# Performance work log

Hardware: AMD Instinct MI355X
Metric: run time of the kernel (lower is better)

Reference implementation:

```python
import jax, jax.numpy as jnp
import numpy as np

B, F, NQ, DT, TS, K = 16384, 256, 2048, 256, 16, 8
GH, SH, CALH = 128, 128, 16
SPD = DT + TS
SPH = max(int(SPD * 0.25), 16)
CD = DT + 3 + TS + 3  # h_base + y_base + 3 gate stats + z_top + |d_safe| + |d_spec| = 278
CH = max(int(CD * 0.25), 16)
RES_SCALE = 0.1


def _ln(x, g, b):
    m = x.mean(-1, keepdims=True)
    v = ((x - m) ** 2).mean(-1, keepdims=True)
    return (x - m) * jax.lax.rsqrt(v + 1e-5) * g + b


def _resmlp(x, lg, lb, w1, b1, w2, b2):
    h = jnp.maximum(_ln(x, lg, lb) @ w1 + b1, 0.0)
    return h @ w2 + b2


def setup_inputs() -> dict:
    key = jax.random.key(0)
    ks = iter(jax.random.split(key, 48))
    def nrm(shape, s=0.05):
        return jax.random.normal(next(ks), shape, jnp.float32) * s
    d = {}
    d["x_num"] = jax.random.normal(next(ks), (B, F), jnp.float32)
    d["robust_center"] = nrm((1, F), 0.1)
    d["robust_scale"] = jax.random.uniform(next(ks), (1, F), jnp.float32, 0.5, 1.5)
    d["quantile_sorted"] = jnp.sort(jax.random.normal(next(ks), (NQ, F), jnp.float32), axis=0)
    d["stem_w1"] = nrm((3, CALH)); d["stem_b1"] = jnp.zeros((CALH,))
    d["stem_w2"] = nrm((CALH, CALH)); d["stem_b2"] = jnp.zeros((CALH,))
    d["stem_w3"] = nrm((CALH, 1)); d["stem_b3"] = jnp.zeros((1,))
    d["gate_w1"] = nrm((F, GH)); d["gate_b1"] = jnp.zeros((GH,))
    d["gate_w2"] = nrm((GH, F)); d["gate_b2"] = jnp.zeros((F,))
    d["bb_w"] = nrm((F, DT)); d["bb_b"] = jnp.zeros((DT,))
    d["base_w"] = nrm((DT, 1)); d["base_b"] = jnp.zeros((1,))
    d["safe_lg"] = jnp.ones((DT,)); d["safe_lb"] = jnp.zeros((DT,))
    d["safe_w1"] = nrm((DT, SH)); d["safe_b1"] = jnp.zeros((SH,))
    d["safe_w2"] = nrm((SH, 1)); d["safe_b2"] = jnp.zeros((1,))
    d["top_w1"] = nrm((1, TS)); d["top_b1"] = jnp.zeros((TS,))
    d["top_w2"] = nrm((TS, TS)); d["top_b2"] = jnp.zeros((TS,))
    d["spec_lg"] = jnp.ones((SPD,)); d["spec_lb"] = jnp.zeros((SPD,))
    d["spec_w1"] = nrm((SPD, SPH)); d["spec_b1"] = jnp.zeros((SPH,))
    d["spec_w2"] = nrm((SPH, 1)); d["spec_b2"] = jnp.zeros((1,))
    d["conf_lg"] = jnp.ones((CD,)); d["conf_lb"] = jnp.zeros((CD,))
    d["conf_w1"] = nrm((CD, CH)); d["conf_b1"] = jnp.zeros((CH,))
    d["conf_w2"] = nrm((CH, 1)); d["conf_b2"] = jnp.full((1,), -2.0)  # gamma_init_bias
    return d


def _forward(x_num, robust_center, robust_scale, quantile_sorted,
             stem_w1, stem_b1, stem_w2, stem_b2, stem_w3, stem_b3,
             gate_w1, gate_b1, gate_w2, gate_b2,
             bb_w, bb_b, base_w, base_b,
             safe_lg, safe_lb, safe_w1, safe_b1, safe_w2, safe_b2,
             top_w1, top_b1, top_w2, top_b2,
             spec_lg, spec_lb, spec_w1, spec_b1, spec_w2, spec_b2,
             conf_lg, conf_lb, conf_w1, conf_b1, conf_w2, conf_b2):
    # --- calibration views ---
    x_robust = (x_num - robust_center) / robust_scale
    ranks = jax.vmap(jnp.searchsorted, in_axes=(1, 1), out_axes=1)(
        jax.lax.stop_gradient(quantile_sorted), jax.lax.stop_gradient(x_num))  # [B,F] int
    x_quant = jnp.clip(ranks.astype(jnp.float32) / (NQ - 1.0), 0.0, 1.0)
    x_views = jnp.stack([x_num, x_robust, x_quant], axis=-1)  # [B,F,3]
    h = jnp.maximum(x_views @ stem_w1 + stem_b1, 0.0)
    h = jnp.maximum(h @ stem_w2 + stem_b2, 0.0)
    resid = jnp.tanh((h @ stem_w3 + stem_b3)[..., 0])
    x_cal = x_num + RES_SCALE * resid
    # --- input gate ---
    g = jax.nn.sigmoid(jnp.maximum(x_cal @ gate_w1 + gate_b1, 0.0) @ gate_w2 + gate_b2)
    x_gated = x_cal * g
    # --- backbone (stand-in for TMLPBackbone.encode_hidden) ---
    h_base = jnp.maximum(x_gated @ bb_w + bb_b, 0.0)  # [B,DT]
    y_base = h_base @ base_w + base_b  # [B,1]
    gate_mean = g.mean(axis=1, keepdims=True)
    gate_max = g.max(axis=1, keepdims=True)
    gate_std = g.std(axis=1, keepdims=True)  # ddof=0, matches unbiased=False
    delta_safe = _resmlp(h_base, safe_lg, safe_lb, safe_w1, safe_b1, safe_w2, safe_b2)
    # --- top-k feature gather ---
    topk_g, topk_idx = jax.lax.top_k(g, K)
    topk_x = jnp.take_along_axis(x_cal, topk_idx, axis=1)
    topk_w = topk_g / (topk_g.sum(axis=1, keepdims=True) + 1e-6)
    xw = (topk_x * topk_w)[..., None]  # [B,K,1]
    tok = jnp.maximum(xw @ top_w1 + top_b1, 0.0) @ top_w2 + top_b2  # [B,K,TS]
    z_top = tok.mean(axis=1)  # [B,TS]
    delta_spec = _resmlp(jnp.concatenate([h_base, z_top], axis=1),
                         spec_lg, spec_lb, spec_w1, spec_b1, spec_w2, spec_b2)
    conf_in = jnp.concatenate([h_base, y_base, gate_mean, gate_max, gate_std,
                               z_top, jnp.abs(delta_safe), jnp.abs(delta_spec)], axis=1)
    gamma = jax.nn.sigmoid(_resmlp(conf_in, conf_lg, conf_lb, conf_w1, conf_b1, conf_w2, conf_b2))
    return (y_base + delta_safe + gamma * delta_spec)[:, 0]


def reference(x_num, robust_center, robust_scale, quantile_sorted,
              stem_w1, stem_b1, stem_w2, stem_b2, stem_w3, stem_b3,
              gate_w1, gate_b1, gate_w2, gate_b2,
              bb_w, bb_b, base_w, base_b,
              safe_lg, safe_lb, safe_w1, safe_b1, safe_w2, safe_b2,
              top_w1, top_b1, top_w2, top_b2,
              spec_lg, spec_lb, spec_w1, spec_b1, spec_w2, spec_b2,
              conf_lg, conf_lb, conf_w1, conf_b1, conf_w2, conf_b2):
    return _forward(x_num, robust_center, robust_scale, quantile_sorted,
                    stem_w1, stem_b1, stem_w2, stem_b2, stem_w3, stem_b3,
                    gate_w1, gate_b1, gate_w2, gate_b2,
                    bb_w, bb_b, base_w, base_b,
                    safe_lg, safe_lb, safe_w1, safe_b1, safe_w2, safe_b2,
                    top_w1, top_b1, top_w2, top_b2,
                    spec_lg, spec_lb, spec_w1, spec_b1, spec_w2, spec_b2,
                    conf_lg, conf_lb, conf_w1, conf_b1, conf_w2, conf_b2)
```

## Files before the change

kernel.cpp:

```cpp
#include <hip/hip_runtime.h>
#include <hip/hip_bf16.h>
#include <math.h>

static constexpr int B  = 16384;
static constexpr int F  = 256;
static constexpr int NQ = 2048;
static constexpr int TS = 16;
static constexpr int KTOP = 8;
static constexpr int SPD = 272;
static constexpr int SPH = 68;
static constexpr int CD  = 278;
static constexpr int CH  = 69;

typedef __attribute__((ext_vector_type(8))) short bf16x8;
typedef __attribute__((ext_vector_type(4))) float f32x4;
typedef _Float16 f16x2 __attribute__((ext_vector_type(2)));
typedef unsigned u32x4 __attribute__((ext_vector_type(4)));

__device__ inline short f2bf(float f) {
    unsigned u = __builtin_bit_cast(unsigned, f);
    unsigned r = (u + 0x7FFF + ((u >> 16) & 1)) >> 16;
    return (short)r;
}

__device__ inline unsigned pkbf(float a, float b) {
    __hip_bfloat162 h = __float22bfloat162_rn(make_float2(a, b));
    unsigned u;
    __builtin_memcpy(&u, &h, 4);
    return u;
}

__device__ inline float fast_tanh(float o) {
    o = fminf(fmaxf(o, -15.0f), 15.0f);
    float e = __expf(2.0f * o);
    return (e - 1.0f) / (e + 1.0f);
}

__device__ inline f16x2 cvt2h(float a, float b) {
    return __builtin_bit_cast(f16x2, __builtin_amdgcn_cvt_pkrtz(a, b));
}

__device__ inline unsigned pack2h(float a, float b) {
    return __builtin_bit_cast(unsigned, __builtin_amdgcn_cvt_pkrtz(a, b));
}

__device__ inline void prep_one(const float* W, short* T, int local,
                                int K, int N, int KP) {
    const int n = local / KP, k = local - n * KP;
    T[local] = (k < K && n < N) ? f2bf(W[k * N + n]) : (short)0;
}

__global__ __launch_bounds__(256) void k_prepall(
    const float* __restrict__ gate_w1, const float* __restrict__ gate_w2,
    const float* __restrict__ bb_w,    const float* __restrict__ safe_w1,
    const float* __restrict__ spec_w1, const float* __restrict__ conf_w1,
    const float* __restrict__ qs,
    const float* __restrict__ stem_w2, const float* __restrict__ stem_w3,
    short* __restrict__ w1t, short* __restrict__ w2t, short* __restrict__ bbt,
    short* __restrict__ sw1t, short* __restrict__ spw1t, short* __restrict__ cfw1t,
    float* __restrict__ qs_t,
    unsigned* __restrict__ w2ph, unsigned* __restrict__ w3ph)
{
    __shared__ float tile[64][65];
    if (blockIdx.x < 929) {
        const int idx = blockIdx.x * 256 + threadIdx.x;
        if (idx < 32768)       prep_one(gate_w1, w1t,  idx,           256, 128, 256);
        else if (idx < 65536)  prep_one(gate_w2, w2t,  idx - 32768,   128, 256, 128);
        else if (idx < 131072) prep_one(bb_w,    bbt,  idx - 65536,   256, 256, 256);
        else if (idx < 163840) prep_one(safe_w1, sw1t, idx - 131072,  256, 128, 256);
        else if (idx < 200704) prep_one(spec_w1, spw1t, idx - 163840, 272, 68, 288);
        else if (idx < 237568) prep_one(conf_w1, cfw1t, idx - 200704, 278, 69, 288);
        else if (idx < 237696) {
            const int l = idx - 237568;
            const int t = l >> 4, j = l & 15;
            w2ph[l] = pack2h(stem_w2[(2 * t) * 16 + j], stem_w2[(2 * t + 1) * 16 + j]);
        }
        else if (idx < 237704) {
            const int u = idx - 237696;
            w3ph[u] = pack2h(stem_w3[2 * u], stem_w3[2 * u + 1]);
        }
    } else {
        const int t = blockIdx.x - 929;
        const int tq = t & 31, tf = t >> 5;
        const int q0 = tq * 64, f0 = tf * 64;
        const int c = threadIdx.x & 63, r4 = threadIdx.x >> 6;
#pragma unroll
        for (int rr = 0; rr < 16; ++rr) {
            const int row = rr * 4 + r4;
            tile[row][c] = qs[(q0 + row) * 256 + f0 + c];
        }
        __syncthreads();
#pragma unroll
        for (int rr = 0; rr < 16; ++rr) {
            const int fr = rr * 4 + r4;
            qs_t[(long)(f0 + fr) * 2048 + q0 + c] = tile[c][fr];
        }
    }
}

__global__ __launch_bounds__(256) void k_calib7(
    const float* __restrict__ x_num, const float* __restrict__ center,
    const float* __restrict__ scale, const float* __restrict__ qs,
    const float* __restrict__ qs_t,
    const float* __restrict__ sw1, const float* __restrict__ sb1,
    const unsigned* __restrict__ w2ph, const float* __restrict__ sb2,
    const unsigned* __restrict__ w3ph, const float* __restrict__ sb3,
    float* __restrict__ x_cal)
{
    __shared__ float cq[63 * 256];
    const int tid = threadIdx.x;
    const int f = tid;
#pragma unroll 1
    for (int j0 = 0; j0 < 63; j0 += 9) {
        float t[9];
#pragma unroll
        for (int u = 0; u < 9; ++u) t[u] = qs[(32 * (j0 + u + 1)) * 256 + tid];
#pragma unroll
        for (int u = 0; u < 9; ++u) cq[(j0 + u) * 256 + tid] = t[u];
    }
    __syncthreads();

    const float c = center[f];
    const float inv_sc = 1.0f / scale[f];
    const float* colp = qs_t + (long)f * NQ;
    const long row_base = (long)blockIdx.x * 32;

    float xb[8];
#pragma unroll
    for (int i = 0; i < 8; ++i) xb[i] = x_num[(row_base + i) * F + f];

#pragma unroll
    for (int grp = 0; grp < 4; ++grp) {
        const long r0 = row_base + grp * 8;
        float x[8], xr[8];
#pragma unroll
        for (int i = 0; i < 8; ++i) x[i] = xb[i];
        if (grp < 3) {
#pragma unroll
            for (int i = 0; i < 8; ++i) xb[i] = x_num[(r0 + 8 + i) * F + f];
        }
#pragma unroll
        for (int i = 0; i < 8; ++i) xr[i] = (x[i] - c) * inv_sc;

        int lo[8], hi[8];
#pragma unroll
        for (int i = 0; i < 8; ++i) { lo[i] = 0; hi[i] = 63; }
#pragma unroll
        for (int it = 0; it < 6; ++it) {
            float qv[8]; int mid[8];
#pragma unroll
            for (int i = 0; i < 8; ++i) {
                mid[i] = (lo[i] + hi[i]) >> 1;
                qv[i] = cq[mid[i] * 256 + f];
            }
#pragma unroll
            for (int i = 0; i < 8; ++i) {
                if (qv[i] < x[i]) lo[i] = mid[i] + 1; else hi[i] = mid[i];
            }
        }
        int base[8];
        {
            float pm[8];
#pragma unroll
            for (int i = 0; i < 8; ++i) pm[i] = colp[lo[i] * 32 + 16];
#pragma unroll
            for (int i = 0; i < 8; ++i)
                base[i] = lo[i] * 32 + ((pm[i] < x[i]) ? 16 : 0);
        }
        float xq[8];
#pragma unroll
        for (int i = 0; i < 8; ++i) {
            const float4* wp = reinterpret_cast<const float4*>(&colp[base[i]]);
            const float4 a = wp[0], b = wp[1], d = wp[2], e = wp[3];
            int cN = 0;
            cN += (a.x < x[i]); cN += (a.y < x[i]); cN += (a.z < x[i]); cN += (a.w < x[i]);
            cN += (b.x < x[i]); cN += (b.y < x[i]); cN += (b.z < x[i]); cN += (b.w < x[i]);
            cN += (d.x < x[i]); cN += (d.y < x[i]); cN += (d.z < x[i]); cN += (d.w < x[i]);
            cN += (e.x < x[i]); cN += (e.y < x[i]); cN += (e.z < x[i]); cN += (e.w < x[i]);
            const int rank = base[i] + cN;
            xq[i] = fminf((float)rank * (1.0f / (float)(NQ - 1)), 1.0f);
        }

#pragma unroll
        for (int hgrp = 0; hgrp < 2; ++hgrp) {
            const int o4 = hgrp * 4;
            float h2[4][16];
#pragma unroll
            for (int j = 0; j < 16; ++j) {
                const float bb = sb2[j];
#pragma unroll
                for (int i = 0; i < 4; ++i) h2[i][j] = bb;
            }
#pragma unroll 4
            for (int t = 0; t < 8; ++t) {
                const float w0a = sw1[2 * t],     w1a = sw1[16 + 2 * t],     w2a = sw1[32 + 2 * t];
                const float w0b = sw1[2 * t + 1], w1b = sw1[16 + 2 * t + 1], w2b = sw1[32 + 2 * t + 1];
                const float ba = sb1[2 * t], bbv = sb1[2 * t + 1];
                f16x2 hp[4];
#pragma unroll
                for (int i = 0; i < 4; ++i) {
                    const float ha = fmaxf(ba  + x[o4 + i] * w0a + xr[o4 + i] * w1a + xq[o4 + i] * w2a, 0.0f);
                    const float hb = fmaxf(bbv + x[o4 + i] * w0b + xr[o4 + i] * w1b + xq[o4 + i] * w2b, 0.0f);
                    hp[i] = cvt2h(ha, hb);
                }
                unsigned ww[16];
                const uint4* wr = reinterpret_cast<const uint4*>(&w2ph[t * 16]);
                *reinterpret_cast<uint4*>(&ww[0])  = wr[0];
                *reinterpret_cast<uint4*>(&ww[4])  = wr[1];
                *reinterpret_cast<uint4*>(&ww[8])  = wr[2];
                *reinterpret_cast<uint4*>(&ww[12]) = wr[3];
#pragma unroll
                for (int j = 0; j < 16; ++j) {
                    const f16x2 wj = __builtin_bit_cast(f16x2, ww[j]);
#pragma unroll
                    for (int i = 0; i < 4; ++i)
                        h2[i][j] = __builtin_amdgcn_fdot2(hp[i], wj, h2[i][j], false);
                }
            }
            const float b3 = sb3[0];
            float o[4] = {b3, b3, b3, b3};
#pragma unroll
            for (int u = 0; u < 8; ++u) {
                const f16x2 wu = __builtin_bit_cast(f16x2, w3ph[u]);
#pragma unroll
                for (int i = 0; i < 4; ++i) {
                    const f16x2 hh = cvt2h(
                        fmaxf(h2[i][2 * u], 0.0f), fmaxf(h2[i][2 * u + 1], 0.0f));
                    o[i] = __builtin_amdgcn_fdot2(hh, wu, o[i], false);
                }
            }
#pragma unroll
            for (int i = 0; i < 4; ++i)
                x_cal[(r0 + o4 + i) * F + f] = x[o4 + i] + 0.1f * fast_tanh(o[i]);
        }
    }
}

static constexpr int ST1 = 136;
static constexpr int ST2 = 264;

__global__ __launch_bounds__(256) void k_fused(
    const float* __restrict__ x_cal,
    const short* __restrict__ w1t, const float* __restrict__ gate_b1,
    const short* __restrict__ w2t, const float* __restrict__ gate_b2,
    const short* __restrict__ bbt, const float* __restrict__ bb_b,
    float* __restrict__ g, float* __restrict__ h_b)
{
    __shared__ short s_c1[32 * ST1];
    __shared__ short s_xg[32 * ST2];

    const int tid = threadIdx.x;
    const int wave = tid >> 6, lane = tid & 63;
    const int sub = lane & 15, quad = lane >> 4;
    const int wm = wave & 1, wn = wave >> 1;
    const long row0 = (long)blockIdx.x * 32;
    const long mrow = row0 + wm * 16 + sub;

    {
        f32x4 acc[4];
#pragma unroll
        for (int t = 0; t < 4; ++t) acc[t] = (f32x4){0, 0, 0, 0};
#pragma unroll
        for (int k0 = 0; k0 < 256; k0 += 32) {
            const float* ap = x_cal + mrow * 256 + k0 + quad * 8;
            float av[8];
            *reinterpret_cast<float4*>(&av[0]) = *reinterpret_cast<const float4*>(ap);
            *reinterpret_cast<float4*>(&av[4]) = *reinterpret_cast<const float4*>(ap + 4);
            u32x4 afu;
            afu[0] = pkbf(av[0], av[1]);
            afu[1] = pkbf(av[2], av[3]);
            afu[2] = pkbf(av[4], av[5]);
            afu[3] = pkbf(av[6], av[7]);
            const bf16x8 af = __builtin_bit_cast(bf16x8, afu);
#pragma unroll
            for (int t = 0; t < 4; ++t) {
                const int col = wn * 64 + t * 16 + sub;
                const bf16x8 bf = *reinterpret_cast<const bf16x8*>(
                    &w1t[(long)col * 256 + k0 + quad * 8]);
                acc[t] = __builtin_amdgcn_mfma_f32_16x16x32_bf16(af, bf, acc[t], 0, 0, 0);
            }
        }
#pragma unroll
        for (int t = 0; t < 4; ++t) {
            const int col = wn * 64 + t * 16 + sub;
            const float bb = gate_b1[col];
#pragma unroll
            for (int r = 0; r < 4; ++r) {
                const int rowl = wm * 16 + quad * 4 + r;
                s_c1[rowl * ST1 + col] = f2bf(fmaxf(acc[t][r] + bb, 0.0f));
            }
        }
    }
    __syncthreads();

    {
        f32x4 acc[8];
#pragma unroll
        for (int t = 0; t < 8; ++t) acc[t] = (f32x4){0, 0, 0, 0};
#pragma unroll
        for (int k0 = 0; k0 < 128; k0 += 32) {
            const bf16x8 af = *reinterpret_cast<const bf16x8*>(
                &s_c1[(wm * 16 + sub) * ST1 + k0 + quad * 8]);
#pragma unroll
            for (int t = 0; t < 8; ++t) {
                const int col = wn * 128 + t * 16 + sub;
                const bf16x8 bf = *reinterpret_cast<const bf16x8*>(
                    &w2t[(long)col * 128 + k0 + quad * 8]);
                acc[t] = __builtin_amdgcn_mfma_f32_16x16x32_bf16(af, bf, acc[t], 0, 0, 0);
            }
        }
#pragma unroll
        for (int t = 0; t < 8; ++t) {
            const int col = wn * 128 + t * 16 + sub;
            const float bb = gate_b2[col];
#pragma unroll
            for (int r = 0; r < 4; ++r) {
                const int rowl = wm * 16 + quad * 4 + r;
                const float gv = 1.0f / (1.0f + __expf(-(acc[t][r] + bb)));
                g[(row0 + rowl) * 256 + col] = gv;
                const float xg = x_cal[(row0 + rowl) * 256 + col] * gv;
                s_xg[rowl * ST2 + col] = f2bf(xg);
            }
        }
    }
    __syncthreads();

    {
        f32x4 acc[8];
#pragma unroll
        for (int t = 0; t < 8; ++t) acc[t] = (f32x4){0, 0, 0, 0};
#pragma unroll
        for (int k0 = 0; k0 < 256; k0 += 32) {
            const bf16x8 af = *reinterpret_cast<const bf16x8*>(
                &s_xg[(wm * 16 + sub) * ST2 + k0 + quad * 8]);
#pragma unroll
            for (int t = 0; t < 8; ++t) {
                const int col = wn * 128 + t * 16 + sub;
                const bf16x8 bf = *reinterpret_cast<const bf16x8*>(
                    &bbt[(long)col * 256 + k0 + quad * 8]);
                acc[t] = __builtin_amdgcn_mfma_f32_16x16x32_bf16(af, bf, acc[t], 0, 0, 0);
            }
        }
#pragma unroll
        for (int t = 0; t < 8; ++t) {
            const int col = wn * 128 + t * 16 + sub;
            const float bb = bb_b[col];
#pragma unroll
            for (int r = 0; r < 4; ++r) {
                const int rowl = wm * 16 + quad * 4 + r;
                h_b[(row0 + rowl) * 256 + col] = fmaxf(acc[t][r] + bb, 0.0f);
            }
        }
    }
}

__global__ __launch_bounds__(256) void k_topk(
    const float* __restrict__ g, const float* __restrict__ x_cal,
    const float* __restrict__ tw1, const float* __restrict__ tb1,
    const float* __restrict__ tw2, const float* __restrict__ tb2,
    float* __restrict__ z_top, float* __restrict__ stats)
{
    __shared__ float s_hm[4][16];
    const int wave = threadIdx.x >> 6;
    const int lane = threadIdx.x & 63;
    const int b = blockIdx.x * 4 + wave;
    const long base = (long)b * F;

    float gv[4];
#pragma unroll
    for (int i = 0; i < 4; ++i) gv[i] = g[base + lane + 64 * i];

    float s = gv[0] + gv[1] + gv[2] + gv[3];
    float mx = fmaxf(fmaxf(gv[0], gv[1]), fmaxf(gv[2], gv[3]));
    for (int m = 32; m; m >>= 1) {
        s  += __shfl_xor(s, m);
        mx  = fmaxf(mx, __shfl_xor(mx, m));
    }
    const float mean = s * (1.0f / 256.0f);
    float vs = 0.0f;
#pragma unroll
    for (int i = 0; i < 4; ++i) { float d = gv[i] - mean; vs += d * d; }
    for (int m = 32; m; m >>= 1) vs += __shfl_xor(vs, m);
    const float stdv = sqrtf(vs * (1.0f / 256.0f));

    float cur[4]; int curi[4];
#pragma unroll
    for (int i = 0; i < 4; ++i) { cur[i] = gv[i]; curi[i] = lane + 64 * i; }
    float tv[KTOP]; int ti[KTOP]; float vsum = 0.0f;
    for (int r = 0; r < KTOP; ++r) {
        float bv = cur[0]; int bi = curi[0];
#pragma unroll
        for (int i = 1; i < 4; ++i)
            if (cur[i] > bv || (cur[i] == bv && curi[i] < bi)) { bv = cur[i]; bi = curi[i]; }
        for (int m = 32; m; m >>= 1) {
            float ov = __shfl_xor(bv, m);
            int   oi = __shfl_xor(bi, m);
            if (ov > bv || (ov == bv && oi < bi)) { bv = ov; bi = oi; }
        }
        tv[r] = bv; ti[r] = bi; vsum += bv;
#pragma unroll
        for (int i = 0; i < 4; ++i) if (curi[i] == bi) cur[i] = -INFINITY;
    }
    const float denom = 1.0f / (vsum + 1e-6f);

    if (lane < 16) {
        float hm = 0.0f;
        for (int k = 0; k < KTOP; ++k) {
            const float xk = x_cal[base + ti[k]];
            const float xw = xk * (tv[k] * denom);
            hm += fmaxf(xw * tw1[lane] + tb1[lane], 0.0f);
        }
        s_hm[wave][lane] = hm * (1.0f / (float)KTOP);
    }
    __syncthreads();
    if (lane < 16) {
        float z = tb2[lane];
#pragma unroll
        for (int j = 0; j < 16; ++j) z += s_hm[wave][j] * tw2[j * 16 + lane];
        z_top[(long)b * TS + lane] = z;
    }
    if (lane == 0) {
        stats[(long)b * 4 + 0] = mean;
        stats[(long)b * 4 + 1] = mx;
        stats[(long)b * 4 + 2] = stdv;
    }
}

static constexpr int HST = 260;
static constexpr int AST = 312;

template<int KP>
__device__ __forceinline__ void head_mfma16(
    const short* sa, const short* __restrict__ Wt,
    const float* __restrict__ b1v, const float* __restrict__ w2v, int Nreal,
    float (*s_red)[16], int wave, int sub, int quad)
{
    f32x4 acc[2];
#pragma unroll
    for (int t = 0; t < 2; ++t) acc[t] = (f32x4){0, 0, 0, 0};
#pragma unroll
    for (int k0 = 0; k0 < KP; k0 += 32) {
        const bf16x8 af = *reinterpret_cast<const bf16x8*>(
            &sa[sub * AST + k0 + quad * 8]);
#pragma unroll
        for (int t = 0; t < 2; ++t) {
            const int col = wave * 32 + t * 16 + sub;
            const bf16x8 bf = *reinterpret_cast<const bf16x8*>(
                &Wt[(long)col * KP + k0 + quad * 8]);
            acc[t] = __builtin_amdgcn_mfma_f32_16x16x32_bf16(af, bf, acc[t], 0, 0, 0);
        }
    }
    float rsum[4] = {0, 0, 0, 0};
#pragma unroll
    for (int t = 0; t < 2; ++t) {
        const int col = wave * 32 + t * 16 + sub;
        const float bb = (col < Nreal) ? b1v[col] : 0.0f;
        const float ww = (col < Nreal) ? w2v[col] : 0.0f;
#pragma unroll
        for (int rr = 0; rr < 4; ++rr)
            rsum[rr] += fmaxf(acc[t][rr] + bb, 0.0f) * ww;
    }
#pragma unroll
    for (int rr = 0; rr < 4; ++rr)
        for (int m = 1; m < 16; m <<= 1) rsum[rr] += __shfl_xor(rsum[rr], m);
    if (sub == 0) {
#pragma unroll
        for (int rr = 0; rr < 4; ++rr)
            s_red[wave][quad * 4 + rr] = rsum[rr];
    }
}

__global__ __launch_bounds__(256) void k_tail3(
    const float* __restrict__ h_base, const float* __restrict__ z_top,
    const float* __restrict__ gstats,
    const float* __restrict__ base_w, const float* __restrict__ base_b,
    const float* __restrict__ safe_lg, const float* __restrict__ safe_lb,
    const short* __restrict__ sw1t, const float* __restrict__ safe_b1,
    const float* __restrict__ safe_w2, const float* __restrict__ safe_b2,
    const float* __restrict__ spec_lg, const float* __restrict__ spec_lb,
    const short* __restrict__ spw1t, const float* __restrict__ spec_b1,
    const float* __restrict__ spec_w2, const float* __restrict__ spec_b2,
    const float* __restrict__ conf_lg, const float* __restrict__ conf_lb,
    const short* __restrict__ cfw1t, const float* __restrict__ conf_b1,
    const float* __restrict__ conf_w2, const float* __restrict__ conf_b2,
    float* __restrict__ out)
{
    __shared__ float s_h[16 * HST];
    __shared__ short s_a[16 * AST];
    __shared__ float s_z[16 * 16];
    __shared__ float s_g[16 * 4];
    __shared__ float s_sc[16 * 14];
    __shared__ float s_red[4][16];

    const int tid = threadIdx.x;
    const int wave = tid >> 6, lane = tid & 63;
    const int sub = lane & 15, quad = lane >> 4;
    const long row0 = (long)blockIdx.x * 16;

    for (int idx = tid; idx < 16 * 64; idx += 256) {
        const int r = idx >> 6, q = idx & 63;
        *reinterpret_cast<float4*>(&s_h[r * HST + q * 4]) =
            *reinterpret_cast<const float4*>(&h_base[(row0 + r) * 256 + q * 4]);
    }
    if (tid < 256) s_z[tid] = z_top[row0 * 16 + tid];
    if (tid < 64) s_g[tid] = gstats[row0 * 4 + tid];
    __syncthreads();

    {
        const int r = tid >> 4, l16 = tid & 15;
        float S = 0.0f, SS = 0.0f, Y = 0.0f;
#pragma unroll
        for (int i = 0; i < 16; ++i) {
            const int k = l16 + 16 * i;
            const float v = s_h[r * HST + k];
            S += v; SS += v * v; Y += v * base_w[k];
        }
        const float z0 = s_z[r * 16 + l16];
        float Sz = z0, SSz = z0 * z0;
#pragma unroll
        for (int m = 1; m < 16; m <<= 1) {
            S += __shfl_xor(S, m); SS += __shfl_xor(SS, m); Y += __shfl_xor(Y, m);
            Sz += __shfl_xor(Sz, m); SSz += __shfl_xor(SSz, m);
        }
        if (l16 == 0) {
            float* sc = &s_sc[r * 14];
            sc[0] = S; sc[1] = SS; sc[2] = Sz; sc[3] = SSz;
            sc[4] = Y + base_b[0];
            const float mu = S * (1.0f / 256.0f);
            sc[5] = mu;
            sc[6] = rsqrtf(SS * (1.0f / 256.0f) - mu * mu + 1e-5f);
            const float musp = (S + Sz) * (1.0f / (float)SPD);
            sc[7] = musp;
            sc[8] = rsqrtf((SS + SSz) * (1.0f / (float)SPD) - musp * musp + 1e-5f);
        }
    }
    __syncthreads();

    for (int idx = tid; idx < 16 * 128; idx += 256) {
        const int r = idx >> 7, k = (idx & 127) * 2;
        const float mu = s_sc[r * 14 + 5], rs = s_sc[r * 14 + 6];
        const float v0 = (s_h[r * HST + k] - mu) * rs * safe_lg[k] + safe_lb[k];
        const float v1 = (s_h[r * HST + k + 1] - mu) * rs * safe_lg[k + 1] + safe_lb[k + 1];
        *reinterpret_cast<unsigned*>(&s_a[r * AST + k]) = pkbf(v0, v1);
    }
    __syncthreads();

    head_mfma16<256>(s_a, sw1t, safe_b1, safe_w2, 128, s_red, wave, sub, quad);
    __syncthreads();

    if (tid < 16)
        s_sc[tid * 14 + 9] = s_red[0][tid] + s_red[1][tid] + s_red[2][tid] + s_red[3][tid] + safe_b2[0];
    for (int idx = tid; idx < 16 * 144; idx += 256) {
        const int r = idx / 144, k = (idx - r * 144) * 2;
        const float mu = s_sc[r * 14 + 7], rs = s_sc[r * 14 + 8];
        float vv[2];
#pragma unroll
        for (int h = 0; h < 2; ++h) {
            const int kk = k + h;
            float raw = (kk < 256) ? s_h[r * HST + kk]
                       : (kk < SPD) ? s_z[r * 16 + kk - 256] : 0.0f;
            vv[h] = (kk < SPD) ? (raw - mu) * rs * spec_lg[kk] + spec_lb[kk] : 0.0f;
        }
        *reinterpret_cast<unsigned*>(&s_a[r * AST + k]) = pkbf(vv[0], vv[1]);
    }
    __syncthreads();

    head_mfma16<288>(s_a, spw1t, spec_b1, spec_w2, SPH, s_red, wave, sub, quad);
    __syncthreads();

    if (tid < 16) {
        float* sc = &s_sc[tid * 14];
        const float dsp = s_red[0][tid] + s_red[1][tid] + s_red[2][tid] + s_red[3][tid] + spec_b2[0];
        sc[10] = dsp;
        const float yb = sc[4];
        const float gm = s_g[tid * 4 + 0], gx = s_g[tid * 4 + 1], gs = s_g[tid * 4 + 2];
        const float ads = fabsf(sc[9]), adp = fabsf(dsp);
        const float es = yb + gm + gx + gs + ads + adp;
        const float eq = yb * yb + gm * gm + gx * gx + gs * gs + ads * ads + adp * adp;
        const float muc = (sc[0] + sc[2] + es) * (1.0f / (float)CD);
        sc[11] = muc;
        sc[12] = rsqrtf((sc[1] + sc[3] + eq) * (1.0f / (float)CD) - muc * muc + 1e-5f);
    }
    __syncthreads();

    for (int idx = tid; idx < 16 * 144; idx += 256) {
        const int r = idx / 144, k = (idx - r * 144) * 2;
        const float mu = s_sc[r * 14 + 11], rs = s_sc[r * 14 + 12];
        float vv[2];
#pragma unroll
        for (int h = 0; h < 2; ++h) {
            const int kk = k + h;
            float raw;
            if (kk < 256)       raw = s_h[r * HST + kk];
            else if (kk == 256) raw = s_sc[r * 14 + 4];
            else if (kk == 257) raw = s_g[r * 4 + 0];
            else if (kk == 258) raw = s_g[r * 4 + 1];
            else if (kk == 259) raw = s_g[r * 4 + 2];
            else if (kk < 276)  raw = s_z[r * 16 + kk - 260];
            else if (kk == 276) raw = fabsf(s_sc[r * 14 + 9]);
            else if (kk == 277) raw = fabsf(s_sc[r * 14 + 10]);
            else                raw = 0.0f;
            vv[h] = (kk < CD) ? (raw - mu) * rs * conf_lg[kk] + conf_lb[kk] : 0.0f;
        }
        *reinterpret_cast<unsigned*>(&s_a[r * AST + k]) = pkbf(vv[0], vv[1]);
    }
    __syncthreads();

    head_mfma16<288>(s_a, cfw1t, conf_b1, conf_w2, CH, s_red, wave, sub, quad);
    __syncthreads();

    if (tid < 16) {
        const float* sc = &s_sc[tid * 14];
        const float gamma = 1.0f / (1.0f + __expf(
            -(s_red[0][tid] + s_red[1][tid] + s_red[2][tid] + s_red[3][tid] + conf_b2[0])));
        out[row0 + tid] = sc[4] + sc[9] + gamma * sc[10];
    }
}

extern "C" void kernel_launch(void* const* d_in, const int* in_sizes, int n_in,
                              void* d_out, int out_size, void* d_ws, size_t ws_size,
                              hipStream_t stream)
{
    const float* x_num   = (const float*)d_in[0];
    const float* center  = (const float*)d_in[1];
    const float* scale   = (const float*)d_in[2];
    const float* qs      = (const float*)d_in[3];
    const float* stem_w1 = (const float*)d_in[4];
    const float* stem_b1 = (const float*)d_in[5];
    const float* stem_w2 = (const float*)d_in[6];
    const float* stem_b2 = (const float*)d_in[7];
    const float* stem_w3 = (const float*)d_in[8];
    const float* stem_b3 = (const float*)d_in[9];
    const float* gate_w1 = (const float*)d_in[10];
    const float* gate_b1 = (const float*)d_in[11];
    const float* gate_w2 = (const float*)d_in[12];
    const float* gate_b2 = (const float*)d_in[13];
    const float* bb_w    = (const float*)d_in[14];
    const float* bb_b    = (const float*)d_in[15];
    const float* base_w  = (const float*)d_in[16];
    const float* base_b  = (const float*)d_in[17];
    const float* safe_lg = (const float*)d_in[18];
    const float* safe_lb = (const float*)d_in[19];
    const float* safe_w1 = (const float*)d_in[20];
    const float* safe_b1 = (const float*)d_in[21];
    const float* safe_w2 = (const float*)d_in[22];
    const float* safe_b2 = (const float*)d_in[23];
    const float* top_w1  = (const float*)d_in[24];
    const float* top_b1  = (const float*)d_in[25];
    const float* top_w2  = (const float*)d_in[26];
    const float* top_b2  = (const float*)d_in[27];
    const float* spec_lg = (const float*)d_in[28];
    const float* spec_lb = (const float*)d_in[29];
    const float* spec_w1 = (const float*)d_in[30];
    const float* spec_b1 = (const float*)d_in[31];
    const float* spec_w2 = (const float*)d_in[32];
    const float* spec_b2 = (const float*)d_in[33];
    const float* conf_lg = (const float*)d_in[34];
    const float* conf_lb = (const float*)d_in[35];
    const float* conf_w1 = (const float*)d_in[36];
    const float* conf_b1 = (const float*)d_in[37];
    const float* conf_w2 = (const float*)d_in[38];
    const float* conf_b2 = (const float*)d_in[39];

    float* ws    = (float*)d_ws;
    float* x_cal = ws;
    float* g_h   = x_cal + (long)B * 256;
    float* g     = g_h   + (long)B * 128;
    float* h_b   = g     + (long)B * 256;
    float* z_top = h_b   + (long)B * 256;
    float* gstat = z_top + (long)B * 16;
    short* w1t   = (short*)(gstat + (long)B * 4);
    short* w2t   = w1t   + 128 * 256;
    short* bbt   = w2t   + 256 * 128;
    short* sw1t  = bbt   + 256 * 256;
    short* spw1t = sw1t  + 128 * 256;
    short* cfw1t = spw1t + 128 * 288;
    unsigned* w2ph = (unsigned*)(cfw1t + 128 * 288);
    unsigned* w3ph = w2ph + 128;
    float* qs_t  = (float*)(w3ph + 8);
    float* out   = (float*)d_out;

    k_prepall<<<1057, 256, 0, stream>>>(gate_w1, gate_w2, bb_w, safe_w1, spec_w1,
                                        conf_w1, qs, stem_w2, stem_w3,
                                        w1t, w2t, bbt, sw1t, spw1t, cfw1t, qs_t,
                                        w2ph, w3ph);
    k_calib7<<<512, 256, 0, stream>>>(x_num, center, scale, qs, qs_t,
                                      stem_w1, stem_b1, w2ph, stem_b2, w3ph, stem_b3,
                                      x_cal);
    k_fused<<<512, 256, 0, stream>>>(x_cal, w1t, gate_b1, w2t, gate_b2, bbt, bb_b,
                                     g, h_b);
    k_topk<<<B / 4, 256, 0, stream>>>(g, x_cal, top_w1, top_b1, top_w2, top_b2, z_top, gstat);
    k_tail3<<<B / 16, 256, 0, stream>>>(h_b, z_top, gstat,
                                        base_w, base_b,
                                        safe_lg, safe_lb, sw1t, safe_b1, safe_w2, safe_b2,
                                        spec_lg, spec_lb, spw1t, spec_b1, spec_w2, spec_b2,
                                        conf_lg, conf_lb, cfw1t, conf_b1, conf_w2, conf_b2,
                                        out);
}
```

Measured before the change: 354.3 us.

## Fuse top-k gate statistics into the gate/backbone GEMM kernel

Removes the separate k_topk launch and runs its per-row gate stats, top-k selection and top-feature MLP at the end of the fused gate/backbone kernel. Each of the four waves handles eight of the block's 32 rows, and the LDS round trip for hm is replaced by a wave shuffle. This saves one launch and lets g be re-read while likely still in cache, but the top-k work now runs serially on only 512 blocks. It also stops unrolling the group loop in the calibration kernel, probably to reduce register pressure, at the cost of losing some overlap from the prefetch.

New measurement: 323.0 us. 8.8% less time.

```diff
diff --git a/kernel.cpp b/kernel.cpp
--- a/kernel.cpp
+++ b/kernel.cpp
@@ -129,7 +129,7 @@
 #pragma unroll
     for (int i = 0; i < 8; ++i) xb[i] = x_num[(row_base + i) * F + f];
 
-#pragma unroll
+#pragma unroll 1
     for (int grp = 0; grp < 4; ++grp) {
         const long r0 = row_base + grp * 8;
         float x[8], xr[8];
@@ -239,12 +239,15 @@
 static constexpr int ST1 = 136;
 static constexpr int ST2 = 264;
 
-__global__ __launch_bounds__(256) void k_fused(
+__global__ __launch_bounds__(256) void k_fused2(
     const float* __restrict__ x_cal,
     const short* __restrict__ w1t, const float* __restrict__ gate_b1,
     const short* __restrict__ w2t, const float* __restrict__ gate_b2,
     const short* __restrict__ bbt, const float* __restrict__ bb_b,
-    float* __restrict__ g, float* __restrict__ h_b)
+    const float* __restrict__ tw1, const float* __restrict__ tb1,
+    const float* __restrict__ tw2, const float* __restrict__ tb2,
+    float* __restrict__ g, float* __restrict__ h_b,
+    float* __restrict__ z_top, float* __restrict__ stats)
 {
     __shared__ short s_c1[32 * ST1];
     __shared__ short s_xg[32 * ST2];
@@ -352,77 +355,70 @@
             }
         }
     }
-}
-
-__global__ __launch_bounds__(256) void k_topk(
-    const float* __restrict__ g, const float* __restrict__ x_cal,
-    const float* __restrict__ tw1, const float* __restrict__ tb1,
-    const float* __restrict__ tw2, const float* __restrict__ tb2,
-    float* __restrict__ z_top, float* __restrict__ stats)
-{
-    __shared__ float s_hm[4][16];
-    const int wave = threadIdx.x >> 6;
-    const int lane = threadIdx.x & 63;
-    const int b = blockIdx.x * 4 + wave;
-    const long base = (long)b * F;
-
-    float gv[4];
-#pragma unroll
-    for (int i = 0; i < 4; ++i) gv[i] = g[base + lane + 64 * i];
-
-    float s = gv[0] + gv[1] + gv[2] + gv[3];
-    float mx = fmaxf(fmaxf(gv[0], gv[1]), fmaxf(gv[2], gv[3]));
-    for (int m = 32; m; m >>= 1) {
-        s  += __shfl_xor(s, m);
-        mx  = fmaxf(mx, __shfl_xor(mx, m));
-    }
-    const float mean = s * (1.0f / 256.0f);
-    float vs = 0.0f;
-#pragma unroll
-    for (int i = 0; i < 4; ++i) { float d = gv[i] - mean; vs += d * d; }
-    for (int m = 32; m; m >>= 1) vs += __shfl_xor(vs, m);
-    const float stdv = sqrtf(vs * (1.0f / 256.0f));
-
-    float cur[4]; int curi[4];
-#pragma unroll
-    for (int i = 0; i < 4; ++i) { cur[i] = gv[i]; curi[i] = lane + 64 * i; }
-    float tv[KTOP]; int ti[KTOP]; float vsum = 0.0f;
-    for (int r = 0; r < KTOP; ++r) {
-        float bv = cur[0]; int bi = curi[0];
-#pragma unroll
-        for (int i = 1; i < 4; ++i)
-            if (cur[i] > bv || (cur[i] == bv && curi[i] < bi)) { bv = cur[i]; bi = curi[i]; }
+
+#pragma unroll 1
+    for (int jr = 0; jr < 8; ++jr) {
+        const int r = wave * 8 + jr;
+        const long bb = row0 + r;
+        float gv[4];
+#pragma unroll
+        for (int i = 0; i < 4; ++i) gv[i] = g[bb * 256 + lane + 64 * i];
+
+        float s = gv[0] + gv[1] + gv[2] + gv[3];
+        float mx = fmaxf(fmaxf(gv[0], gv[1]), fmaxf(gv[2], gv[3]));
         for (int m = 32; m; m >>= 1) {
-            float ov = __shfl_xor(bv, m);
-            int   oi = __shfl_xor(bi, m);
-            if (ov > bv || (ov == bv && oi < bi)) { bv = ov; bi = oi; }
-        }
-        tv[r] = bv; ti[r] = bi; vsum += bv;
-#pragma unroll
-        for (int i = 0; i < 4; ++i) if (curi[i] == bi) cur[i] = -INFINITY;
-    }
-    const float denom = 1.0f / (vsum + 1e-6f);
-
-    if (lane < 16) {
+            s  += __shfl_xor(s, m);
+            mx  = fmaxf(mx, __shfl_xor(mx, m));
+        }
+        const float mean = s * (1.0f / 256.0f);
+        float vs = 0.0f;
+#pragma unroll
+        for (int i = 0; i < 4; ++i) { float d = gv[i] - mean; vs += d * d; }
+        for (int m = 32; m; m >>= 1) vs += __shfl_xor(vs, m);
+        const float stdv = sqrtf(vs * (1.0f / 256.0f));
+
+        float cur[4]; int curi[4];
+#pragma unroll
+        for (int i = 0; i < 4; ++i) { cur[i] = gv[i]; curi[i] = lane + 64 * i; }
+        float tv[KTOP]; int ti[KTOP]; float vsum = 0.0f;
+#pragma unroll
+        for (int rr = 0; rr < KTOP; ++rr) {
+            float bv = cur[0]; int bi = curi[0];
+#pragma unroll
+            for (int i = 1; i < 4; ++i)
+                if (cur[i] > bv || (cur[i] == bv && curi[i] < bi)) { bv = cur[i]; bi = curi[i]; }
+            for (int m = 32; m; m >>= 1) {
+                float ov = __shfl_xor(bv, m);
+                int   oi = __shfl_xor(bi, m);
+                if (ov > bv || (ov == bv && oi < bi)) { bv = ov; bi = oi; }
+            }
+            tv[rr] = bv; ti[rr] = bi; vsum += bv;
+#pragma unroll
+            for (int i = 0; i < 4; ++i) if (curi[i] == bi) cur[i] = -INFINITY;
+        }
+        const float denom = 1.0f / (vsum + 1e-6f);
+
         float hm = 0.0f;
-        for (int k = 0; k < KTOP; ++k) {
-            const float xk = x_cal[base + ti[k]];
-            const float xw = xk * (tv[k] * denom);
-            hm += fmaxf(xw * tw1[lane] + tb1[lane], 0.0f);
-        }
-        s_hm[wave][lane] = hm * (1.0f / (float)KTOP);
-    }
-    __syncthreads();
-    if (lane < 16) {
-        float z = tb2[lane];
-#pragma unroll
-        for (int j = 0; j < 16; ++j) z += s_hm[wave][j] * tw2[j * 16 + lane];
-        z_top[(long)b * TS + lane] = z;
-    }
-    if (lane == 0) {
-        stats[(long)b * 4 + 0] = mean;
-        stats[(long)b * 4 + 1] = mx;
-        stats[(long)b * 4 + 2] = stdv;
+        if (lane < 16) {
+#pragma unroll
+            for (int k = 0; k < KTOP; ++k) {
+                const float xk = x_cal[bb * 256 + ti[k]];
+                const float xw = xk * (tv[k] * denom);
+                hm += fmaxf(xw * tw1[lane] + tb1[lane], 0.0f);
+            }
+            hm *= (1.0f / (float)KTOP);
+        }
+        if (lane < 16) {
+            float z = tb2[lane];
+#pragma unroll
+            for (int j = 0; j < 16; ++j) z += __shfl(hm, j) * tw2[j * 16 + lane];
+            z_top[bb * TS + lane] = z;
+        }
+        if (lane == 0) {
+            stats[bb * 4 + 0] = mean;
+            stats[bb * 4 + 1] = mx;
+            stats[bb * 4 + 2] = stdv;
+        }
     }
 }
 
@@ -687,9 +683,9 @@
     k_calib7<<<512, 256, 0, stream>>>(x_num, center, scale, qs, qs_t,
                                       stem_w1, stem_b1, w2ph, stem_b2, w3ph, stem_b3,
                                       x_cal);
-    k_fused<<<512, 256, 0, stream>>>(x_cal, w1t, gate_b1, w2t, gate_b2, bbt, bb_b,
-                                     g, h_b);
-    k_topk<<<B / 4, 256, 0, stream>>>(g, x_cal, top_w1, top_b1, top_w2, top_b2, z_top, gstat);
+    k_fused2<<<512, 256, 0, stream>>>(x_cal, w1t, gate_b1, w2t, gate_b2, bbt, bb_b,
+                                      top_w1, top_b1, top_w2, top_b2,
+                                      g, h_b, z_top, gstat);
     k_tail3<<<B / 16, 256, 0, stream>>>(h_b, z_top, gstat,
                                         base_w, base_b,
                                         safe_lg, safe_lb, sw1t, safe_b1, safe_w2, safe_b2,
```
